# Kernel tuning notes

Measured on AMD Instinct MI355X. Metric: run time of the kernel, lower is better.

Reference implementation:

```python
import jax, jax.numpy as jnp
import numpy as np

N_DEST, N_SRC = 8192, 8192
FEAT, TFD, EMB, HID, HEADS = 1024, 256, 64, 128, 2
NEG_INF = -9e15


def setup_inputs() -> dict:
    key = jax.random.key(0)
    ks = jax.random.split(key, 8)
    bias = (jax.random.uniform(ks[0], (N_DEST, N_SRC)) < 0.01).astype(jnp.float32)
    emb_dest = jax.random.normal(ks[1], (N_DEST, EMB), jnp.float32)
    emb_src = jax.random.normal(ks[2], (N_SRC, EMB), jnp.float32)
    feature_src = jax.random.normal(ks[3], (N_SRC, FEAT), jnp.float32)
    scale = 0.05
    fc_W = jax.random.normal(ks[4], (TFD, FEAT), jnp.float32) * scale
    fc_b = jnp.zeros((TFD,), jnp.float32)
    dec_W = jax.random.normal(ks[5], (FEAT, TFD), jnp.float32) * scale
    dec_b = jnp.zeros((FEAT,), jnp.float32)
    att_W = jax.random.normal(ks[6], (HEADS, EMB, HID), jnp.float32) * scale
    att_W2 = jax.random.normal(ks[7], (HEADS, HID, HID), jnp.float32) * scale
    return dict(bias=bias, emb_dest=emb_dest, emb_src=emb_src,
                feature_src=feature_src, fc_W=fc_W, fc_b=fc_b,
                dec_W=dec_W, dec_b=dec_b, att_W=att_W, att_W2=att_W2)


def reference(bias, emb_dest, emb_src, feature_src, fc_W, fc_b, dec_W, dec_b, att_W, att_W2):
    # encoder: [N_src, FEAT] -> [N_src, TFD]
    transformed = feature_src @ fc_W.T + fc_b
    # per-head projections of node embeddings: h = emb @ W  -> [H, N, HID]
    h_src = jnp.einsum('ne,hed->hnd', emb_src, att_W)
    h_dst = jnp.einsum('me,hed->hmd', emb_dest, att_W)
    # e = elu((h_dst @ W2) @ h_src^T)  -> [H, N_dest, N_src]
    scores = jax.nn.elu(jnp.einsum('hmd,hdk,hnk->hmn', h_dst, att_W2, h_src))
    masked = jnp.where(bias > 0, scores, NEG_INF)
    attn = jax.nn.softmax(masked, axis=-1)  # row-wise over source nodes
    # aggregate transformed source features, mean over heads -> [N_dest, TFD]
    feature_src_re = jnp.einsum('hmn,nf->hmf', attn, transformed).mean(axis=0)
    # decoder (autoencoder reconstruction): [N_src, FEAT]
    feature_hat = transformed @ dec_W.T + dec_b
    return feature_src_re, feature_hat
```

## Files before the change

kernel.cpp:

```cpp
#include <hip/hip_runtime.h>
#include <hip/hip_bf16.h>

#define N_DEST 8192
#define N_SRC  8192
#define FEATD  1024
#define TFDIM  256
#define EMBD   64
#define HIDD   128
#define LDO    1024
#define CAP 1024
#define LSTRIDE 256
#define SCAP 240

typedef float  f32x4  __attribute__((ext_vector_type(4)));
typedef __bf16 bf16x8 __attribute__((ext_vector_type(8)));
typedef unsigned short u16x4 __attribute__((ext_vector_type(4)));

__device__ inline bf16x8 load8cvt(const float* p) {
  const f32x4 u = *(const f32x4*)p;
  const f32x4 v = *(const f32x4*)(p + 4);
  bf16x8 r;
  #pragma unroll
  for (int i = 0; i < 4; ++i) { r[i] = (__bf16)u[i]; r[i + 4] = (__bf16)v[i]; }
  return r;
}
__device__ inline unsigned short bfbits(float f) {
  __bf16 b = (__bf16)f;
  return *(unsigned short*)&b;
}
__device__ inline float bf2f(unsigned short u) {
  union { unsigned int i; float f; } x;
  x.i = (unsigned int)u << 16;
  return x.f;
}

__global__ __launch_bounds__(256) void gemm_mfma_k1(
    const float* __restrict__ A, const float* __restrict__ B,
    const float* __restrict__ bias, float* __restrict__ stage,
    unsigned short* __restrict__ apack)
{
  const int wave = threadIdx.x >> 6, lane = threadIdx.x & 63;
  const int l15 = lane & 15, quad = lane >> 4;
  const int row0 = blockIdx.x * 64 + wave * 16;
  const int col0 = blockIdx.y * 64;

  const float* Ap = A + (size_t)(row0 + l15) * FEATD + quad * 8;
  const float* Bp = B + (size_t)(col0 + l15) * FEATD + quad * 8;

  f32x4 acc[4];
  #pragma unroll
  for (int i = 0; i < 4; ++i) acc[i] = (f32x4){0.f, 0.f, 0.f, 0.f};

  for (int k = 0; k < FEATD; k += 32) {
    const bf16x8 a  = load8cvt(Ap + k);
    const bf16x8 b0 = load8cvt(Bp + k);
    const bf16x8 b1 = load8cvt(Bp + (size_t)16 * FEATD + k);
    const bf16x8 b2 = load8cvt(Bp + (size_t)32 * FEATD + k);
    const bf16x8 b3 = load8cvt(Bp + (size_t)48 * FEATD + k);
    acc[0] = __builtin_amdgcn_mfma_f32_16x16x32_bf16(a, b0, acc[0], 0, 0, 0);
    acc[1] = __builtin_amdgcn_mfma_f32_16x16x32_bf16(a, b1, acc[1], 0, 0, 0);
    acc[2] = __builtin_amdgcn_mfma_f32_16x16x32_bf16(a, b2, acc[2], 0, 0, 0);
    acc[3] = __builtin_amdgcn_mfma_f32_16x16x32_bf16(a, b3, acc[3], 0, 0, 0);
  }

  #pragma unroll
  for (int ct = 0; ct < 4; ++ct) {
    const int n = col0 + ct * 16 + l15;
    const float bn = bias[n];
    #pragma unroll
    for (int r = 0; r < 4; ++r) {
      const int mm = row0 + quad * 4 + r;
      const float v = acc[ct][r] + bn;
      const unsigned short pb = bfbits(v);
      stage[(size_t)mm * LDO + n] = v;
      ((unsigned short*)(stage + (size_t)mm * LDO + 768))[n] = pb;
      if (apack) apack[(size_t)mm * TFDIM + n] = pb;
    }
  }
}

__global__ __launch_bounds__(128) void proj_all(
    const float* __restrict__ emb_src, const float* __restrict__ emb_dest,
    const float* __restrict__ att_W, const float* __restrict__ att_W2,
    float* __restrict__ stage)
{
  const int t = threadIdx.x;
  const int b = blockIdx.x;
  const int rb    = b & 511;
  const int h     = (b >> 9) & 1;
  const int which = b >> 10;
  const int row0  = rb * 16;

  __shared__ float se[16][EMBD];
  __shared__ float hh[16][HIDD];

  const float* e = (which ? emb_dest : emb_src) + (size_t)row0 * EMBD;
  for (int i = t; i < 16 * EMBD; i += 128) se[i >> 6][i & 63] = e[i];
  __syncthreads();

  float acc[16];
  #pragma unroll
  for (int r = 0; r < 16; ++r) acc[r] = 0.f;
  const float* W = att_W + (size_t)h * EMBD * HIDD + t;
  for (int d = 0; d < EMBD; ++d) {
    const float w = W[d * HIDD];
    #pragma unroll
    for (int r = 0; r < 16; ++r) acc[r] += se[r][d] * w;
  }

  if (!which) {
    #pragma unroll
    for (int r = 0; r < 16; ++r) {
      const size_t row = row0 + r;
      stage[row * LDO + 256 + h * HIDD + t] = acc[r];
      ((unsigned short*)(stage + row * LDO + 896))[h * HIDD + t] = bfbits(acc[r]);
    }
    return;
  }

  #pragma unroll
  for (int r = 0; r < 16; ++r) hh[r][t] = acc[r];
  __syncthreads();

  float g[16];
  #pragma unroll
  for (int r = 0; r < 16; ++r) g[r] = 0.f;
  const float* W2 = att_W2 + (size_t)h * HIDD * HIDD + t;
  for (int d = 0; d < HIDD; ++d) {
    const float w2 = W2[d * HIDD];
    #pragma unroll
    for (int r = 0; r < 16; ++r) g[r] += hh[r][d] * w2;
  }
  #pragma unroll
  for (int r = 0; r < 16; ++r)
    stage[(size_t)(row0 + r) * LDO + 512 + h * HIDD + t] = g[r];
}

__global__ __launch_bounds__(256) void extract_nbrs(
    const float* __restrict__ bias, int* __restrict__ counts,
    int* __restrict__ lists)
{
  const int m = blockIdx.x;
  __shared__ int cnt;
  __shared__ int buf[CAP];
  if (threadIdx.x == 0) cnt = 0;
  __syncthreads();
  const float* brow = bias + (size_t)m * N_SRC;
  for (int base = threadIdx.x * 4; base < N_SRC; base += 1024) {
    const f32x4 v = *(const f32x4*)(brow + base);
    #pragma unroll
    for (int e = 0; e < 4; ++e)
      if (v[e] > 0.f) {
        const int p = atomicAdd(&cnt, 1);
        if (p < CAP) buf[p] = base + e;
      }
  }
  __syncthreads();
  const int c = cnt;
  if (threadIdx.x == 0) counts[m] = c;
  int lim = c < LSTRIDE ? c : LSTRIDE;
  for (int t = threadIdx.x; t < lim; t += 256)
    lists[(size_t)m * LSTRIDE + t] = buf[t];
}

__global__ __launch_bounds__(256, 4) void attn_gather(
    const float* __restrict__ bias, const float* __restrict__ stage,
    const int* __restrict__ counts, const int* __restrict__ lists,
    float* __restrict__ out)
{
  const int m = blockIdx.x;
  const int tid = threadIdx.x;
  const int lane = tid & 63, wv = tid >> 6;

  __shared__ float g0[HIDD], g1[HIDD];
  __shared__ float s0[256], s1[256];
  __shared__ int   lidx[256];
  __shared__ float rA[4], rB[4];
  __shared__ float p0[4][TFDIM], p1[4][TFDIM];

  const float* gs = stage + (size_t)m * LDO + 512;
  if (tid < 128) { g0[tid] = gs[tid]; g1[tid] = gs[HIDD + tid]; }
  const int count = counts[m];
  __syncthreads();

  if (count > 0 && count <= SCAP) {
    const int countPad = (count + 15) & ~15;
    if (tid < countPad)
      lidx[tid] = (tid < count) ? lists[(size_t)m * LSTRIDE + tid] : 0;
    __syncthreads();

    const int grp = tid >> 3, r8 = tid & 7;
    for (int t0 = 0; t0 < count; t0 += 32) {
      const int t = t0 + grp;
      float q0 = 0.f, q1 = 0.f;
      if (t < count) {
        const int j = lidx[t];
        const __bf16* hb = (const __bf16*)(stage + (size_t)j * LDO + 896);
        const bf16x8 x0 = *(const bf16x8*)(hb + r8 * 16);
        const bf16x8 x1 = *(const bf16x8*)(hb + r8 * 16 + 8);
        const bf16x8 y0 = *(const bf16x8*)(hb + HIDD + r8 * 16);
        const bf16x8 y1 = *(const bf16x8*)(hb + HIDD + r8 * 16 + 8);
        #pragma unroll
        for (int e = 0; e < 8; ++e) {
          q0 += g0[r8 * 16 + e]     * (float)x0[e];
          q0 += g0[r8 * 16 + 8 + e] * (float)x1[e];
          q1 += g1[r8 * 16 + e]     * (float)y0[e];
          q1 += g1[r8 * 16 + 8 + e] * (float)y1[e];
        }
      }
      #pragma unroll
      for (int off = 1; off < 8; off <<= 1) {
        q0 += __shfl_xor(q0, off);
        q1 += __shfl_xor(q1, off);
      }
      if (r8 == 0 && t < count) {
        s0[t] = (q0 > 0.f) ? q0 : expm1f(q0);
        s1[t] = (q1 > 0.f) ? q1 : expm1f(q1);
      }
    }
    __syncthreads();

    float m0 = (tid < count) ? s0[tid] : -3.4e38f;
    float m1 = (tid < count) ? s1[tid] : -3.4e38f;
    #pragma unroll
    for (int off = 32; off; off >>= 1) {
      m0 = fmaxf(m0, __shfl_xor(m0, off));
      m1 = fmaxf(m1, __shfl_xor(m1, off));
    }
    if (lane == 0) { rA[wv] = m0; rB[wv] = m1; }
    __syncthreads();
    const float M0 = fmaxf(fmaxf(rA[0], rA[1]), fmaxf(rA[2], rA[3]));
    const float M1 = fmaxf(fmaxf(rB[0], rB[1]), fmaxf(rB[2], rB[3]));
    __syncthreads();

    float w0 = 0.f, w1 = 0.f;
    if (tid < count) {
      w0 = __expf(s0[tid] - M0);
      w1 = __expf(s1[tid] - M1);
    }
    if (tid < countPad) { s0[tid] = w0; s1[tid] = w1; }
    float l0 = w0, l1 = w1;
    #pragma unroll
    for (int off = 32; off; off >>= 1) {
      l0 += __shfl_xor(l0, off);
      l1 += __shfl_xor(l1, off);
    }
    if (lane == 0) { rA[wv] = l0; rB[wv] = l1; }
    __syncthreads();
    const float L0 = rA[0] + rA[1] + rA[2] + rA[3];
    const float L1 = rB[0] + rB[1] + rB[2] + rB[3];

    float b0[4] = {0.f, 0.f, 0.f, 0.f};
    float b1[4] = {0.f, 0.f, 0.f, 0.f};
    const int c4 = lane << 2;
    for (int t = wv << 2; t < countPad; t += 16) {
      #pragma unroll
      for (int q = 0; q < 4; ++q) {
        const int j = lidx[t + q];
        const float u0 = s0[t + q], u1 = s1[t + q];
        const u16x4 tv = *(const u16x4*)(
            (const unsigned short*)(stage + (size_t)j * LDO + 768) + c4);
        #pragma unroll
        for (int i = 0; i < 4; ++i) {
          const float f = bf2f(tv[i]);
          b0[i] += u0 * f;
          b1[i] += u1 * f;
        }
      }
    }
    #pragma unroll
    for (int i = 0; i < 4; ++i) {
      p0[wv][c4 + i] = b0[i];
      p1[wv][c4 + i] = b1[i];
    }
    __syncthreads();
    const float A0 = p0[0][tid] + p0[1][tid] + p0[2][tid] + p0[3][tid];
    const float A1 = p1[0][tid] + p1[1][tid] + p1[2][tid] + p1[3][tid];
    out[(size_t)m * TFDIM + tid] = 0.5f * (A0 / L0 + A1 / L1);
    return;
  }

  float* w0s = (float*)p0[0];
  float* w1s = (float*)p0[1];
  const int c = tid;
  float a0 = 0.f, a1 = 0.f;
  float M0 = -3.4e38f, M1 = -3.4e38f, L0 = 0.f, L1 = 0.f;
  for (int j0 = 0; j0 < N_SRC; j0 += 256) {
    const int j = j0 + tid;
    const float* hb = stage + (size_t)j * LDO + 256;
    float q0 = 0.f, q1 = 0.f;
    for (int d = 0; d < HIDD; d += 4) {
      const f32x4 x = *(const f32x4*)(hb + d);
      const f32x4 y = *(const f32x4*)(hb + HIDD + d);
      #pragma unroll
      for (int e = 0; e < 4; ++e) {
        q0 += g0[d + e] * x[e];
        q1 += g1[d + e] * y[e];
      }
    }
    const bool nz = bias[(size_t)m * N_SRC + j] > 0.f;
    const float sc0 = nz ? ((q0 > 0.f) ? q0 : expm1f(q0)) : -9e15f;
    const float sc1 = nz ? ((q1 > 0.f) ? q1 : expm1f(q1)) : -9e15f;

    float cm0 = sc0, cm1 = sc1;
    #pragma unroll
    for (int off = 32; off; off >>= 1) {
      cm0 = fmaxf(cm0, __shfl_xor(cm0, off));
      cm1 = fmaxf(cm1, __shfl_xor(cm1, off));
    }
    if (lane == 0) { rA[wv] = cm0; rB[wv] = cm1; }
    __syncthreads();
    const float CM0 = fmaxf(fmaxf(rA[0], rA[1]), fmaxf(rA[2], rA[3]));
    const float CM1 = fmaxf(fmaxf(rB[0], rB[1]), fmaxf(rB[2], rB[3]));
    __syncthreads();

    const float nM0 = fmaxf(M0, CM0), nM1 = fmaxf(M1, CM1);
    const float r0 = __expf(M0 - nM0), r1 = __expf(M1 - nM1);
    const float w0 = __expf(sc0 - nM0), w1 = __expf(sc1 - nM1);
    w0s[tid] = w0; w1s[tid] = w1;
    float cl0 = w0, cl1 = w1;
    #pragma unroll
    for (int off = 32; off; off >>= 1) {
      cl0 += __shfl_xor(cl0, off);
      cl1 += __shfl_xor(cl1, off);
    }
    if (lane == 0) { rA[wv] = cl0; rB[wv] = cl1; }
    __syncthreads();
    L0 = L0 * r0 + (rA[0] + rA[1] + rA[2] + rA[3]);
    L1 = L1 * r1 + (rB[0] + rB[1] + rB[2] + rB[3]);
    M0 = nM0; M1 = nM1;
    a0 *= r0; a1 *= r1;
    for (int t2 = 0; t2 < 256; ++t2) {
      const float tv = stage[(size_t)(j0 + t2) * LDO + c];
      a0 += w0s[t2] * tv;
      a1 += w1s[t2] * tv;
    }
    __syncthreads();
  }
  out[(size_t)m * TFDIM + c] = 0.5f * (a0 / L0 + a1 / L1);
}

__global__ __launch_bounds__(64) void attn_stream(
    const float* __restrict__ bias, const float* __restrict__ stage,
    float* __restrict__ out)
{
  const int lane = threadIdx.x;
  const int m = blockIdx.x;
  const int c0 = lane * 4;

  __shared__ float g0[HIDD], g1[HIDD];
  __shared__ int   ring[256];
  __shared__ float wb0[64], wb1[64];

  const float* gs = stage + (size_t)m * LDO + 512;
  g0[lane]      = gs[lane];
  g0[lane + 64] = gs[lane + 64];
  g1[lane]      = gs[HIDD + lane];
  g1[lane + 64] = gs[HIDD + lane + 64];
  __syncthreads();

  float O0[4] = {0.f, 0.f, 0.f, 0.f};
  float O1[4] = {0.f, 0.f, 0.f, 0.f};
  float M0 = -3.4e38f, M1 = -3.4e38f;
  float L0 = 0.f, L1 = 0.f;

  auto flush = [&](int b, int rp) {
    __syncthreads();
    int j = -1;
    if (lane < b) j = ring[(rp + lane) & 255];
    float s0 = 0.f, s1 = 0.f;
    if (j >= 0) {
      const float* h0 = stage + (size_t)j * LDO + 256;
      const float* h1 = h0 + HIDD;
      #pragma unroll
      for (int d = 0; d < HIDD; d += 4) {
        const f32x4 a = *(const f32x4*)(h0 + d);
        const f32x4 c = *(const f32x4*)(h1 + d);
        #pragma unroll
        for (int e = 0; e < 4; ++e) {
          s0 += g0[d + e] * a[e];
          s1 += g1[d + e] * c[e];
        }
      }
      s0 = (s0 > 0.f) ? s0 : expm1f(s0);
      s1 = (s1 > 0.f) ? s1 : expm1f(s1);
    }
    float m0 = (j >= 0) ? s0 : -3.4e38f;
    float m1 = (j >= 0) ? s1 : -3.4e38f;
    #pragma unroll
    for (int off = 32; off; off >>= 1) {
      m0 = fmaxf(m0, __shfl_xor(m0, off));
      m1 = fmaxf(m1, __shfl_xor(m1, off));
    }
    const float nM0 = fmaxf(M0, m0), nM1 = fmaxf(M1, m1);
    const float w0 = (j >= 0) ? __expf(s0 - nM0) : 0.f;
    const float w1 = (j >= 0) ? __expf(s1 - nM1) : 0.f;
    float l0 = w0, l1 = w1;
    #pragma unroll
    for (int off = 32; off; off >>= 1) {
      l0 += __shfl_xor(l0, off);
      l1 += __shfl_xor(l1, off);
    }
    const float r0 = __expf(M0 - nM0);
    const float r1 = __expf(M1 - nM1);
    L0 = L0 * r0 + l0;  L1 = L1 * r1 + l1;
    M0 = nM0;  M1 = nM1;
    #pragma unroll
    for (int i = 0; i < 4; ++i) { O0[i] *= r0; O1[i] *= r1; }
    wb0[lane] = w0;  wb1[lane] = w1;
    __syncthreads();
    for (int n = 0; n < b; ++n) {
      const int jj = ring[(rp + n) & 255];
      const float wa = wb0[n], wc = wb1[n];
      const f32x4 tv = *(const f32x4*)(stage + (size_t)jj * LDO + c0);
      #pragma unroll
      for (int i = 0; i < 4; ++i) {
        O0[i] += wa * tv[i];
        O1[i] += wc * tv[i];
      }
    }
    __syncthreads();
  };

  const float* brow = bias + (size_t)m * N_SRC;
  int wpos = 0, rpos = 0;
  for (int base = 0; base < N_SRC; base += 256) {
    const f32x4 v = *(const f32x4*)(brow + base + lane * 4);
    #pragma unroll
    for (int e = 0; e < 4; ++e) {
      const bool nz = v[e] > 0.f;
      const unsigned long long mask = __ballot(nz);
      if (nz) {
        const int pos = wpos + __popcll(mask & ((1ull << lane) - 1ull));
        ring[pos & 255] = base + lane * 4 + e;
      }
      wpos += __popcll(mask);
      if (wpos - rpos >= 64) { flush(64, rpos); rpos += 64; }
    }
  }
  while (wpos - rpos > 0) {
    const int b = (wpos - rpos < 64) ? (wpos - rpos) : 64;
    flush(b, rpos);
    rpos += b;
  }

  float* orow = out + (size_t)m * TFDIM + c0;
  if (wpos == 0) {
    float o[4] = {0.f, 0.f, 0.f, 0.f};
    for (int j = 0; j < N_SRC; ++j) {
      const f32x4 tv = *(const f32x4*)(stage + (size_t)j * LDO + c0);
      #pragma unroll
      for (int i = 0; i < 4; ++i) o[i] += tv[i];
    }
    const float inv = 1.f / (float)N_SRC;
    #pragma unroll
    for (int i = 0; i < 4; ++i) orow[i] = o[i] * inv;
  } else {
    const float i0 = 1.f / L0, i1 = 1.f / L1;
    #pragma unroll
    for (int i = 0; i < 4; ++i)
      orow[i] = 0.5f * (O0[i] * i0 + O1[i] * i1);
  }
}

__global__ __launch_bounds__(256) void gemm_mfma_dec2(
    const unsigned short* __restrict__ apack,
    const float* __restrict__ W,
    const float* __restrict__ bias,
    float* __restrict__ OUT)
{
  const int wave = threadIdx.x >> 6, lane = threadIdx.x & 63;
  const int l15 = lane & 15, quad = lane >> 4;
  const int row0 = blockIdx.x * 64 + wave * 16;
  const int col0 = blockIdx.y * 64;

  const unsigned short* Ap = apack + (size_t)(row0 + l15) * TFDIM + quad * 8;
  const float* Bp = W + (size_t)(col0 + l15) * TFDIM + quad * 8;

  f32x4 acc[4];
  #pragma unroll
  for (int i = 0; i < 4; ++i) acc[i] = (f32x4){0.f, 0.f, 0.f, 0.f};

  #pragma unroll
  for (int k = 0; k < TFDIM; k += 32) {
    const bf16x8 a  = *(const bf16x8*)(Ap + k);
    const bf16x8 b0 = load8cvt(Bp + k);
    const bf16x8 b1 = load8cvt(Bp + (size_t)16 * TFDIM + k);
    const bf16x8 b2 = load8cvt(Bp + (size_t)32 * TFDIM + k);
    const bf16x8 b3 = load8cvt(Bp + (size_t)48 * TFDIM + k);
    acc[0] = __builtin_amdgcn_mfma_f32_16x16x32_bf16(a, b0, acc[0], 0, 0, 0);
    acc[1] = __builtin_amdgcn_mfma_f32_16x16x32_bf16(a, b1, acc[1], 0, 0, 0);
    acc[2] = __builtin_amdgcn_mfma_f32_16x16x32_bf16(a, b2, acc[2], 0, 0, 0);
    acc[3] = __builtin_amdgcn_mfma_f32_16x16x32_bf16(a, b3, acc[3], 0, 0, 0);
  }

  #pragma unroll
  for (int ct = 0; ct < 4; ++ct) {
    const int n = col0 + ct * 16 + l15;
    const float bn = bias[n];
    #pragma unroll
    for (int r = 0; r < 4; ++r) {
      const int mm = row0 + quad * 4 + r;
      OUT[(size_t)mm * LDO + n] = acc[ct][r] + bn;
    }
  }
}

__global__ __launch_bounds__(128) void gemm_mfma_dec(
    const float* __restrict__ W,
    const float* __restrict__ bias,
    float* __restrict__ OUT)
{
  const int row0 = blockIdx.x * 32;
  const int tid = threadIdx.x;
  const int wave = tid >> 6, lane = tid & 63;
  const int l15 = lane & 15, quad = lane >> 4;

  __shared__ __bf16 Ab[32][TFDIM + 8];

  for (int i = tid; i < 32 * TFDIM; i += 128) {
    const int r = i >> 8, k = i & 255;
    Ab[r][k] = (__bf16)OUT[(size_t)(row0 + r) * LDO + k];
  }
  __syncthreads();

  bf16x8 af[8];
  #pragma unroll
  for (int ks = 0; ks < 8; ++ks)
    af[ks] = *(const bf16x8*)&Ab[wave * 16 + l15][ks * 32 + quad * 8];

  for (int ct = 0; ct < 16; ++ct) {
    f32x4 acc[4];
    #pragma unroll
    for (int i = 0; i < 4; ++i) acc[i] = (f32x4){0.f, 0.f, 0.f, 0.f};
    #pragma unroll
    for (int ks = 0; ks < 8; ++ks) {
      #pragma unroll
      for (int cg = 0; cg < 4; ++cg) {
        const int n = ct * 64 + cg * 16 + l15;
        const bf16x8 bf = load8cvt(W + (size_t)n * TFDIM + ks * 32 + quad * 8);
        acc[cg] = __builtin_amdgcn_mfma_f32_16x16x32_bf16(af[ks], bf, acc[cg], 0, 0, 0);
      }
    }
    #pragma unroll
    for (int cg = 0; cg < 4; ++cg) {
      const int n = ct * 64 + cg * 16 + l15;
      const float bn = bias[n];
      #pragma unroll
      for (int r = 0; r < 4; ++r) {
        const int mm = row0 + wave * 16 + quad * 4 + r;
        OUT[(size_t)mm * LDO + n] = acc[cg][r] + bn;
      }
    }
  }
}

extern "C" void kernel_launch(void* const* d_in, const int* in_sizes, int n_in,
                              void* d_out, int out_size, void* d_ws, size_t ws_size,
                              hipStream_t stream) {
  const float* bias        = (const float*)d_in[0];
  const float* emb_dest    = (const float*)d_in[1];
  const float* emb_src     = (const float*)d_in[2];
  const float* feature_src = (const float*)d_in[3];
  const float* fc_W        = (const float*)d_in[4];
  const float* fc_b        = (const float*)d_in[5];
  const float* dec_W       = (const float*)d_in[6];
  const float* dec_b       = (const float*)d_in[7];
  const float* att_W       = (const float*)d_in[8];
  const float* att_W2      = (const float*)d_in[9];

  float* out0 = (float*)d_out;
  float* out1 = out0 + (size_t)N_DEST * TFDIM;

  const size_t lists_bytes = (size_t)N_DEST * LSTRIDE * sizeof(int);
  const size_t apack_bytes = (size_t)N_SRC * TFDIM * sizeof(unsigned short);
  const size_t need = (size_t)65536 + lists_bytes + apack_bytes;
  const bool use_ws = (ws_size >= need);
  int* counts = (int*)d_ws;
  int* lists  = (int*)((char*)d_ws + 65536);
  unsigned short* apack =
      (unsigned short*)((char*)d_ws + 65536 + lists_bytes);

  {
    dim3 grid(N_SRC / 64, TFDIM / 64);
    gemm_mfma_k1<<<grid, 256, 0, stream>>>(feature_src, fc_W, fc_b, out1,
                                           use_ws ? apack : (unsigned short*)nullptr);
  }
  proj_all<<<2048, 128, 0, stream>>>(emb_src, emb_dest, att_W, att_W2, out1);
  if (use_ws) {
    extract_nbrs<<<N_DEST, 256, 0, stream>>>(bias, counts, lists);
    attn_gather<<<N_DEST, 256, 0, stream>>>(bias, out1, counts, lists, out0);
  } else {
    attn_stream<<<N_DEST, 64, 0, stream>>>(bias, out1, out0);
  }
  if (use_ws) {
    dim3 grid(N_SRC / 64, FEATD / 64);
    gemm_mfma_dec2<<<grid, 256, 0, stream>>>(apack, dec_W, dec_b, out1);
  } else {
    gemm_mfma_dec<<<N_SRC / 32, 128, 0, stream>>>(dec_W, dec_b, out1);
  }
}
```

Measured before the change: 692.3 us.

## Pre-pack weights to bf16, ballot-compact neighbor lists, and regroup score dot products

A new kernel converts fc_W and dec_W to bf16 once per call, so both MFMA GEMMs load packed bf16 B operands instead of converting fp32 on every tile. Neighbor extraction now uses wave ballot with one atomic per wave and writes straight to global lists, dropping the LDS buffer and the copy-out pass. The attention score computation moves from 8 lanes per edge to 4 lanes (per head and half) with a single shuffle, and the kernel order changes so extract_nbrs runs before the GEMM. The extra conversion launch and the extra workspace add overhead. The ballot path also makes list order depend on wave scheduling, which does not change the softmax math.

```diff
diff --git a/kernel.cpp b/kernel.cpp
--- a/kernel.cpp
+++ b/kernel.cpp
@@ -8,7 +8,6 @@
 #define EMBD   64
 #define HIDD   128
 #define LDO    1024
-#define CAP 1024
 #define LSTRIDE 256
 #define SCAP 240
 
@@ -34,10 +33,26 @@
   return x.f;
 }
 
+__global__ __launch_bounds__(256) void cvt_weights(
+    const float* __restrict__ fc_W, const float* __restrict__ dec_W,
+    unsigned short* __restrict__ wpack, unsigned short* __restrict__ dpack)
+{
+  const int which = blockIdx.x >> 8;
+  const int i = ((blockIdx.x & 255) * 256 + threadIdx.x) * 4;
+  const float* src = which ? dec_W : fc_W;
+  unsigned short* dst = which ? dpack : wpack;
+  const f32x4 v = *(const f32x4*)(src + i);
+  u16x4 o;
+  #pragma unroll
+  for (int e = 0; e < 4; ++e) o[e] = bfbits(v[e]);
+  *(u16x4*)(dst + i) = o;
+}
+
 __global__ __launch_bounds__(256) void gemm_mfma_k1(
     const float* __restrict__ A, const float* __restrict__ B,
     const float* __restrict__ bias, float* __restrict__ stage,
-    unsigned short* __restrict__ apack)
+    unsigned short* __restrict__ apack,
+    const unsigned short* __restrict__ wpack)
 {
   const int wave = threadIdx.x >> 6, lane = threadIdx.x & 63;
   const int l15 = lane & 15, quad = lane >> 4;
@@ -45,22 +60,37 @@
   const int col0 = blockIdx.y * 64;
 
   const float* Ap = A + (size_t)(row0 + l15) * FEATD + quad * 8;
-  const float* Bp = B + (size_t)(col0 + l15) * FEATD + quad * 8;
 
   f32x4 acc[4];
   #pragma unroll
   for (int i = 0; i < 4; ++i) acc[i] = (f32x4){0.f, 0.f, 0.f, 0.f};
 
-  for (int k = 0; k < FEATD; k += 32) {
-    const bf16x8 a  = load8cvt(Ap + k);
-    const bf16x8 b0 = load8cvt(Bp + k);
-    const bf16x8 b1 = load8cvt(Bp + (size_t)16 * FEATD + k);
-    const bf16x8 b2 = load8cvt(Bp + (size_t)32 * FEATD + k);
-    const bf16x8 b3 = load8cvt(Bp + (size_t)48 * FEATD + k);
-    acc[0] = __builtin_amdgcn_mfma_f32_16x16x32_bf16(a, b0, acc[0], 0, 0, 0);
-    acc[1] = __builtin_amdgcn_mfma_f32_16x16x32_bf16(a, b1, acc[1], 0, 0, 0);
-    acc[2] = __builtin_amdgcn_mfma_f32_16x16x32_bf16(a, b2, acc[2], 0, 0, 0);
-    acc[3] = __builtin_amdgcn_mfma_f32_16x16x32_bf16(a, b3, acc[3], 0, 0, 0);
+  if (wpack) {
+    const unsigned short* Bq = wpack + (size_t)(col0 + l15) * FEATD + quad * 8;
+    for (int k = 0; k < FEATD; k += 32) {
+      const bf16x8 a  = load8cvt(Ap + k);
+      const bf16x8 b0 = *(const bf16x8*)(Bq + k);
+      const bf16x8 b1 = *(const bf16x8*)(Bq + (size_t)16 * FEATD + k);
+      const bf16x8 b2 = *(const bf16x8*)(Bq + (size_t)32 * FEATD + k);
+      const bf16x8 b3 = *(const bf16x8*)(Bq + (size_t)48 * FEATD + k);
+      acc[0] = __builtin_amdgcn_mfma_f32_16x16x32_bf16(a, b0, acc[0], 0, 0, 0);
+      acc[1] = __builtin_amdgcn_mfma_f32_16x16x32_bf16(a, b1, acc[1], 0, 0, 0);
+      acc[2] = __builtin_amdgcn_mfma_f32_16x16x32_bf16(a, b2, acc[2], 0, 0, 0);
+      acc[3] = __builtin_amdgcn_mfma_f32_16x16x32_bf16(a, b3, acc[3], 0, 0, 0);
+    }
+  } else {
+    const float* Bp = B + (size_t)(col0 + l15) * FEATD + quad * 8;
+    for (int k = 0; k < FEATD; k += 32) {
+      const bf16x8 a  = load8cvt(Ap + k);
+      const bf16x8 b0 = load8cvt(Bp + k);
+      const bf16x8 b1 = load8cvt(Bp + (size_t)16 * FEATD + k);
+      const bf16x8 b2 = load8cvt(Bp + (size_t)32 * FEATD + k);
+      const bf16x8 b3 = load8cvt(Bp + (size_t)48 * FEATD + k);
+      acc[0] = __builtin_amdgcn_mfma_f32_16x16x32_bf16(a, b0, acc[0], 0, 0, 0);
+      acc[1] = __builtin_amdgcn_mfma_f32_16x16x32_bf16(a, b1, acc[1], 0, 0, 0);
+      acc[2] = __builtin_amdgcn_mfma_f32_16x16x32_bf16(a, b2, acc[2], 0, 0, 0);
+      acc[3] = __builtin_amdgcn_mfma_f32_16x16x32_bf16(a, b3, acc[3], 0, 0, 0);
+    }
   }
 
   #pragma unroll
@@ -141,26 +171,29 @@
     int* __restrict__ lists)
 {
   const int m = blockIdx.x;
+  const int tid = threadIdx.x, lane = tid & 63;
   __shared__ int cnt;
-  __shared__ int buf[CAP];
-  if (threadIdx.x == 0) cnt = 0;
+  if (tid == 0) cnt = 0;
   __syncthreads();
   const float* brow = bias + (size_t)m * N_SRC;
-  for (int base = threadIdx.x * 4; base < N_SRC; base += 1024) {
+  int* lrow = lists + (size_t)m * LSTRIDE;
+  for (int base = tid * 4; base < N_SRC; base += 1024) {
     const f32x4 v = *(const f32x4*)(brow + base);
     #pragma unroll
-    for (int e = 0; e < 4; ++e)
-      if (v[e] > 0.f) {
-        const int p = atomicAdd(&cnt, 1);
-        if (p < CAP) buf[p] = base + e;
-      }
+    for (int e = 0; e < 4; ++e) {
+      const bool nz = v[e] > 0.f;
+      const unsigned long long msk = __ballot(nz);
+      int wbase = 0;
+      if (lane == 0 && msk) wbase = atomicAdd(&cnt, __popcll(msk));
+      wbase = __shfl(wbase, 0);
+      if (nz) {
+        const int p = wbase + __popcll(msk & ((1ull << lane) - 1ull));
+        if (p < LSTRIDE) lrow[p] = base + e;
+      }
+    }
   }
   __syncthreads();
-  const int c = cnt;
-  if (threadIdx.x == 0) counts[m] = c;
-  int lim = c < LSTRIDE ? c : LSTRIDE;
-  for (int t = threadIdx.x; t < lim; t += 256)
-    lists[(size_t)m * LSTRIDE + t] = buf[t];
+  if (tid == 0) counts[m] = cnt;
 }
 
 __global__ __launch_bounds__(256, 4) void attn_gather(
@@ -172,14 +205,14 @@
   const int tid = threadIdx.x;
   const int lane = tid & 63, wv = tid >> 6;
 
-  __shared__ float g0[HIDD], g1[HIDD];
+  __shared__ float gq[4][68];
   __shared__ float s0[256], s1[256];
   __shared__ int   lidx[256];
   __shared__ float rA[4], rB[4];
   __shared__ float p0[4][TFDIM], p1[4][TFDIM];
 
   const float* gs = stage + (size_t)m * LDO + 512;
-  if (tid < 128) { g0[tid] = gs[tid]; g1[tid] = gs[HIDD + tid]; }
+  gq[wv][lane] = gs[(wv >> 1) * HIDD + (wv & 1) * 64 + lane];
   const int count = counts[m];
   __syncthreads();
 
@@ -189,33 +222,27 @@
       lidx[tid] = (tid < count) ? lists[(size_t)m * LSTRIDE + tid] : 0;
     __syncthreads();
 
-    const int grp = tid >> 3, r8 = tid & 7;
-    for (int t0 = 0; t0 < count; t0 += 32) {
+    const int grp = tid >> 2, r4 = tid & 3;
+    const int h = r4 >> 1, half = r4 & 1;
+    const float* gh = gq[r4];
+    for (int t0 = 0; t0 < count; t0 += 64) {
       const int t = t0 + grp;
-      float q0 = 0.f, q1 = 0.f;
+      float q = 0.f;
       if (t < count) {
         const int j = lidx[t];
-        const __bf16* hb = (const __bf16*)(stage + (size_t)j * LDO + 896);
-        const bf16x8 x0 = *(const bf16x8*)(hb + r8 * 16);
-        const bf16x8 x1 = *(const bf16x8*)(hb + r8 * 16 + 8);
-        const bf16x8 y0 = *(const bf16x8*)(hb + HIDD + r8 * 16);
-        const bf16x8 y1 = *(const bf16x8*)(hb + HIDD + r8 * 16 + 8);
+        const __bf16* hb =
+            (const __bf16*)(stage + (size_t)j * LDO + 896) + h * HIDD + half * 64;
         #pragma unroll
-        for (int e = 0; e < 8; ++e) {
-          q0 += g0[r8 * 16 + e]     * (float)x0[e];
-          q0 += g0[r8 * 16 + 8 + e] * (float)x1[e];
-          q1 += g1[r8 * 16 + e]     * (float)y0[e];
-          q1 += g1[r8 * 16 + 8 + e] * (float)y1[e];
+        for (int s = 0; s < 8; ++s) {
+          const bf16x8 x = *(const bf16x8*)(hb + s * 8);
+          #pragma unroll
+          for (int e = 0; e < 8; ++e) q += gh[s * 8 + e] * (float)x[e];
         }
       }
-      #pragma unroll
-      for (int off = 1; off < 8; off <<= 1) {
-        q0 += __shfl_xor(q0, off);
-        q1 += __shfl_xor(q1, off);
-      }
-      if (r8 == 0 && t < count) {
-        s0[t] = (q0 > 0.f) ? q0 : expm1f(q0);
-        s1[t] = (q1 > 0.f) ? q1 : expm1f(q1);
+      q += __shfl_xor(q, 1);
+      if (t < count && half == 0) {
+        const float sc = (q > 0.f) ? q : expm1f(q);
+        if (h == 0) s0[t] = sc; else s1[t] = sc;
       }
     }
     __syncthreads();
@@ -290,12 +317,13 @@
     const float* hb = stage + (size_t)j * LDO + 256;
     float q0 = 0.f, q1 = 0.f;
     for (int d = 0; d < HIDD; d += 4) {
+      const int hf = d >> 6, dd = d & 63;
       const f32x4 x = *(const f32x4*)(hb + d);
       const f32x4 y = *(const f32x4*)(hb + HIDD + d);
       #pragma unroll
       for (int e = 0; e < 4; ++e) {
-        q0 += g0[d + e] * x[e];
-        q1 += g1[d + e] * y[e];
+        q0 += gq[hf][dd + e] * x[e];
+        q1 += gq[2 + hf][dd + e] * y[e];
       }
     }
     const bool nz = bias[(size_t)m * N_SRC + j] > 0.f;
@@ -465,7 +493,7 @@
 
 __global__ __launch_bounds__(256) void gemm_mfma_dec2(
     const unsigned short* __restrict__ apack,
-    const float* __restrict__ W,
+    const unsigned short* __restrict__ dpack,
     const float* __restrict__ bias,
     float* __restrict__ OUT)
 {
@@ -475,7 +503,7 @@
   const int col0 = blockIdx.y * 64;
 
   const unsigned short* Ap = apack + (size_t)(row0 + l15) * TFDIM + quad * 8;
-  const float* Bp = W + (size_t)(col0 + l15) * TFDIM + quad * 8;
+  const unsigned short* Bp = dpack + (size_t)(col0 + l15) * TFDIM + quad * 8;
 
   f32x4 acc[4];
   #pragma unroll
@@ -484,10 +512,10 @@
   #pragma unroll
   for (int k = 0; k < TFDIM; k += 32) {
     const bf16x8 a  = *(const bf16x8*)(Ap + k);
-    const bf16x8 b0 = load8cvt(Bp + k);
-    const bf16x8 b1 = load8cvt(Bp + (size_t)16 * TFDIM + k);
-    const bf16x8 b2 = load8cvt(Bp + (size_t)32 * TFDIM + k);
-    const bf16x8 b3 = load8cvt(Bp + (size_t)48 * TFDIM + k);
+    const bf16x8 b0 = *(const bf16x8*)(Bp + k);
+    const bf16x8 b1 = *(const bf16x8*)(Bp + (size_t)16 * TFDIM + k);
+    const bf16x8 b2 = *(const bf16x8*)(Bp + (size_t)32 * TFDIM + k);
+    const bf16x8 b3 = *(const bf16x8*)(Bp + (size_t)48 * TFDIM + k);
     acc[0] = __builtin_amdgcn_mfma_f32_16x16x32_bf16(a, b0, acc[0], 0, 0, 0);
     acc[1] = __builtin_amdgcn_mfma_f32_16x16x32_bf16(a, b1, acc[1], 0, 0, 0);
     acc[2] = __builtin_amdgcn_mfma_f32_16x16x32_bf16(a, b2, acc[2], 0, 0, 0);
@@ -574,28 +602,38 @@
 
   const size_t lists_bytes = (size_t)N_DEST * LSTRIDE * sizeof(int);
   const size_t apack_bytes = (size_t)N_SRC * TFDIM * sizeof(unsigned short);
-  const size_t need = (size_t)65536 + lists_bytes + apack_bytes;
+  const size_t wpack_bytes = (size_t)TFDIM * FEATD * sizeof(unsigned short);
+  const size_t dpack_bytes = (size_t)FEATD * TFDIM * sizeof(unsigned short);
+  const size_t need = 65536 + lists_bytes + apack_bytes + wpack_bytes + dpack_bytes;
   const bool use_ws = (ws_size >= need);
   int* counts = (int*)d_ws;
   int* lists  = (int*)((char*)d_ws + 65536);
-  unsigned short* apack =
-      (unsigned short*)((char*)d_ws + 65536 + lists_bytes);
+  unsigned short* apack = (unsigned short*)((char*)d_ws + 65536 + lists_bytes);
+  unsigned short* wpack = (unsigned short*)((char*)apack + apack_bytes);
+  unsigned short* dpack = (unsigned short*)((char*)wpack + wpack_bytes);
+
+  if (use_ws)
+    cvt_weights<<<512, 256, 0, stream>>>(fc_W, dec_W, wpack, dpack);
+
+  if (use_ws)
+    extract_nbrs<<<N_DEST, 256, 0, stream>>>(bias, counts, lists);
 
   {
     dim3 grid(N_SRC / 64, TFDIM / 64);
-    gemm_mfma_k1<<<grid, 256, 0, stream>>>(feature_src, fc_W, fc_b, out1,
-                                           use_ws ? apack : (unsigned short*)nullptr);
+    gemm_mfma_k1<<<grid, 256, 0, stream>>>(
+        feature_src, fc_W, fc_b, out1,
+        use_ws ? apack : (unsigned short*)nullptr,
+        use_ws ? wpack : (const unsigned short*)nullptr);
   }
   proj_all<<<2048, 128, 0, stream>>>(emb_src, emb_dest, att_W, att_W2, out1);
   if (use_ws) {
-    extract_nbrs<<<N_DEST, 256, 0, stream>>>(bias, counts, lists);
     attn_gather<<<N_DEST, 256, 0, stream>>>(bias, out1, counts, lists, out0);
   } else {
     attn_stream<<<N_DEST, 64, 0, stream>>>(bias, out1, out0);
   }
   if (use_ws) {
     dim3 grid(N_SRC / 64, FEATD / 64);
-    gemm_mfma_dec2<<<grid, 256, 0, stream>>>(apack, dec_W, dec_b, out1);
+    gemm_mfma_dec2<<<grid, 256, 0, stream>>>(apack, dpack, dec_b, out1);
   } else {
     gemm_mfma_dec<<<N_SRC / 32, 128, 0, stream>>>(dec_W, dec_b, out1);
   }
```

Result: faster. 645.5 us (-6.8%).
